# Kernel tuning notes

Hardware: AMD Instinct MI355X
Metric: run time of the kernel (lower is better)

## Reference

```python
import jax, jax.numpy as jnp
import numpy as np

EMBED_DIM = 1024
NUM_HEADS = 16
HEAD_DIM = EMBED_DIM // NUM_HEADS
B, S = 2, 2048


def setup_inputs() -> dict:
    key = jax.random.key(0)
    ks = jax.random.split(key, 11)
    glorot = lambda k, shape: jax.random.normal(k, shape, jnp.float32) * (2.0 / sum(shape)) ** 0.5
    return {
        "query": jax.random.normal(ks[0], (B, S, EMBED_DIM), jnp.float32),
        "key": jax.random.normal(ks[1], (B, S, EMBED_DIM), jnp.float32),
        "value": jax.random.normal(ks[2], (B, S, EMBED_DIM), jnp.float32),
        "Wq": glorot(ks[3], (EMBED_DIM, EMBED_DIM)), "bq": jnp.zeros((EMBED_DIM,), jnp.float32),
        "Wk": glorot(ks[4], (EMBED_DIM, EMBED_DIM)), "bk": jnp.zeros((EMBED_DIM,), jnp.float32),
        "Wv": glorot(ks[5], (EMBED_DIM, EMBED_DIM)), "bv": jnp.zeros((EMBED_DIM,), jnp.float32),
        "Wo": glorot(ks[6], (EMBED_DIM, EMBED_DIM)), "bo": jnp.zeros((EMBED_DIM,), jnp.float32),
    }


def reference(query, key, value, Wq, bq, Wk, bk, Wv, bv, Wo, bo):
    b, s, _ = query.shape
    # QKV projections
    q = query @ Wq + bq
    k = key @ Wk + bk
    v = value @ Wv + bv
    # [B, S, H, D] -> [B, H, S, D]
    q = q.reshape(b, s, NUM_HEADS, HEAD_DIM).transpose(0, 2, 1, 3)
    k = k.reshape(b, s, NUM_HEADS, HEAD_DIM).transpose(0, 2, 1, 3)
    v = v.reshape(b, s, NUM_HEADS, HEAD_DIM).transpose(0, 2, 1, 3)
    # scores [B, H, S, S], materialized as in the original
    scores = jnp.einsum("bhqd,bhkd->bhqk", q, k) / jnp.sqrt(jnp.float32(HEAD_DIM))
    attn = jax.nn.softmax(scores, axis=-1)
    out = jnp.einsum("bhqk,bhkd->bhqd", attn, v)  # [B, H, S, D]
    out = out.transpose(0, 2, 1, 3).reshape(b, s, EMBED_DIM)
    return out @ Wo + bo
```

## Files before the change

### kernel.cpp

```cpp
#include <hip/hip_runtime.h>
#include <hip/hip_bf16.h>


#define EMBED 1024
#define NHEAD 16
#define HDIM 64
#define SEQ 2048
#define MROWS 4096

typedef __attribute__((ext_vector_type(8))) __bf16 bf16x8;
typedef __attribute__((ext_vector_type(4))) float f32x4;
typedef __attribute__((ext_vector_type(16))) float f32x16;

__device__ __forceinline__ unsigned short f2bf(float f) {
  unsigned int u = __builtin_bit_cast(unsigned int, f);
  u += 0x7fffu + ((u >> 16) & 1u);
  return (unsigned short)(u >> 16);
}

__device__ __forceinline__ int cvtpk_bf16(float lo, float hi) {
  int r;
  asm("v_cvt_pk_bf16_f32 %0, %1, %2" : "=v"(r) : "v"(lo), "v"(hi));
  return r;
}

__device__ __forceinline__ float max3f(float a, float b, float c) {
  return fmaxf(fmaxf(a, b), c);
}

__device__ __forceinline__ int swz(int row, int bcol) {
  return row * 128 + (bcol ^ ((row & 7) << 4));
}

__device__ __forceinline__ void gload16(const void* g, void* l) {
  __builtin_amdgcn_global_load_lds((const __attribute__((address_space(1))) void*)g,
                                   (__attribute__((address_space(3))) void*)l, 16, 0, 0);
}

__global__ __launch_bounds__(256) void cvt_f32_bf16(const float* __restrict__ i0, const float* __restrict__ i1,
                                                    const float* __restrict__ i2,
                                                    unsigned short* __restrict__ o0, unsigned short* __restrict__ o1,
                                                    unsigned short* __restrict__ o2) {
  const float* in; unsigned short* out;
  switch (blockIdx.y) {
    case 0: in = i0; out = o0; break;
    case 1: in = i1; out = o1; break;
    default: in = i2; out = o2; break;
  }
  int i = blockIdx.x * 256 + threadIdx.x;
  const float4* p = reinterpret_cast<const float4*>(in) + (size_t)i * 2;
  float4 a = p[0], b = p[1];
  int4 r;
  r.x = cvtpk_bf16(a.x, a.y);
  r.y = cvtpk_bf16(a.z, a.w);
  r.z = cvtpk_bf16(b.x, b.y);
  r.w = cvtpk_bf16(b.z, b.w);
  reinterpret_cast<int4*>(out)[i] = r;
}

__global__ __launch_bounds__(256) void wtrans(const float* __restrict__ w0, const float* __restrict__ w1,
                                              const float* __restrict__ w2, const float* __restrict__ w3,
                                              unsigned short* __restrict__ o0, unsigned short* __restrict__ o1,
                                              unsigned short* __restrict__ o2, unsigned short* __restrict__ o3) {
  __shared__ float tile[64][65];
  const float* src; unsigned short* dst;
  switch (blockIdx.z) {
    case 0: src = w0; dst = o0; break;
    case 1: src = w1; dst = o1; break;
    case 2: src = w2; dst = o2; break;
    default: src = w3; dst = o3; break;
  }
  const int k0 = blockIdx.y * 64, n0 = blockIdx.x * 64;
  const int c = threadIdx.x & 63, r0 = threadIdx.x >> 6;
#pragma unroll
  for (int i = 0; i < 16; ++i) {
    int r = r0 + i * 4;
    tile[r][c] = src[(size_t)(k0 + r) * EMBED + n0 + c];
  }
  __syncthreads();
#pragma unroll
  for (int i = 0; i < 16; ++i) {
    int nr = r0 + i * 4;
    dst[(size_t)(n0 + nr) * EMBED + k0 + c] = f2bf(tile[c][nr]);
  }
}

template <int BN>
__device__ __forceinline__ void gemm_core(const unsigned short* __restrict__ A,
                                          const unsigned short* __restrict__ Bt,
                                          const float* __restrict__ bias,
                                          void* __restrict__ C, float oscale, int mode) {
  constexpr int K = EMBED;
  constexpr int MF = (BN == 128) ? 4 : 2;
  constexpr int BRW = BN / 4;
  __shared__ __align__(16) unsigned short Alds[128 * 64];
  __shared__ __align__(16) unsigned short Blds[BN * 64];
  char* Ab8 = (char*)Alds; char* Bb8 = (char*)Blds;
  const char* AB = (const char*)A;
  const char* BB = (const char*)Bt;
  const int tid = threadIdx.x;
  const int lane = tid & 63, w = tid >> 6;
  const int wr = (BN == 128) ? (w >> 1) : w;
  const int wc = (BN == 128) ? (w & 1) : 0;
  const int fr = lane & 15, fq = lane >> 4;
  const int m0 = blockIdx.y * 128, n0 = blockIdx.x * BN;
  const int bcol = (lane & 7) * 16;
  const int gsc = bcol ^ ((lane >> 3) << 4);

  f32x4 acc[MF][4];
#pragma unroll
  for (int m = 0; m < MF; ++m)
#pragma unroll
    for (int n = 0; n < 4; ++n) acc[m][n] = f32x4{0.f, 0.f, 0.f, 0.f};

  for (int k0 = 0; k0 < K; k0 += 64) {
    __syncthreads();
#pragma unroll
    for (int i = 0; i < 4; ++i) {
      int row = w * 32 + i * 8 + (lane >> 3);
      gload16(AB + (size_t)(m0 + row) * (K * 2) + k0 * 2 + gsc, Ab8 + w * 4096 + i * 1024);
    }
#pragma unroll
    for (int i = 0; i < BRW / 8; ++i) {
      int row = w * BRW + i * 8 + (lane >> 3);
      gload16(BB + (size_t)(n0 + row) * (K * 2) + k0 * 2 + gsc, Bb8 + w * (BRW * 128) + i * 1024);
    }
    __syncthreads();
#pragma unroll
    for (int ks = 0; ks < 2; ++ks) {
      bf16x8 af[MF], bfr[4];
#pragma unroll
      for (int m = 0; m < MF; ++m) {
        int ar = wr * (MF * 16) + m * 16 + fr;
        af[m] = *reinterpret_cast<const bf16x8*>(Ab8 + swz(ar, ks * 64 + fq * 16));
      }
#pragma unroll
      for (int n = 0; n < 4; ++n) {
        int br = wc * 64 + n * 16 + fr;
        bfr[n] = *reinterpret_cast<const bf16x8*>(Bb8 + swz(br, ks * 64 + fq * 16));
      }
#pragma unroll
      for (int m = 0; m < MF; ++m)
#pragma unroll
        for (int n = 0; n < 4; ++n)
          acc[m][n] = __builtin_amdgcn_mfma_f32_16x16x32_bf16(af[m], bfr[n], acc[m][n], 0, 0, 0);
    }
  }

#pragma unroll
  for (int n = 0; n < 4; ++n) {
    int col = n0 + wc * 64 + n * 16 + fr;
    float bv = bias[col];
#pragma unroll
    for (int m = 0; m < MF; ++m) {
      int rowb = m0 + wr * (MF * 16) + m * 16 + fq * 4;
      if (mode == 2) {
        int b = rowb >> 11, s0 = rowb & (SEQ - 1);
        int s0p = (s0 & ~12) | ((s0 & 4) << 1) | ((s0 & 8) >> 1);
        int h = col >> 6, d = col & 63;
        int2 pk;
        pk.x = cvtpk_bf16((acc[m][n][0] + bv) * oscale, (acc[m][n][1] + bv) * oscale);
        pk.y = cvtpk_bf16((acc[m][n][2] + bv) * oscale, (acc[m][n][3] + bv) * oscale);
        *reinterpret_cast<int2*>(
            &reinterpret_cast<unsigned short*>(C)[((size_t)((b * NHEAD + h) * HDIM + d)) * SEQ + s0p]) = pk;
      } else if (mode == 0) {
#pragma unroll
        for (int r = 0; r < 4; ++r) {
          int row = rowb + r;
          float v = (acc[m][n][r] + bv) * oscale;
          int b = row >> 11, s = row & (SEQ - 1), h = col >> 6, d = col & 63;
          reinterpret_cast<unsigned short*>(C)[((size_t)((b * NHEAD + h) * SEQ + s) << 6) + d] = f2bf(v);
        }
      } else {
#pragma unroll
        for (int r = 0; r < 4; ++r)
          reinterpret_cast<float*>(C)[(size_t)(rowb + r) * EMBED + col] = acc[m][n][r] + bv;
      }
    }
  }
}

__global__ __launch_bounds__(256) void gemm_qkv(
    const unsigned short* __restrict__ Xq, const unsigned short* __restrict__ Xk,
    const unsigned short* __restrict__ Xv,
    const unsigned short* __restrict__ Wqt, const unsigned short* __restrict__ Wkt,
    const unsigned short* __restrict__ Wvt,
    const float* __restrict__ bq, const float* __restrict__ bk, const float* __restrict__ bv,
    unsigned short* __restrict__ Qb, unsigned short* __restrict__ Kb,
    unsigned short* __restrict__ Vtb, float qscale) {
  switch (blockIdx.z) {
    case 0: gemm_core<128>(Xq, Wqt, bq, Qb, qscale, 0); break;
    case 1: gemm_core<128>(Xk, Wkt, bk, Kb, 1.0f, 0); break;
    default: gemm_core<128>(Xv, Wvt, bv, Vtb, 1.0f, 2); break;
  }
}

__global__ __launch_bounds__(256) void gemm_out(const unsigned short* __restrict__ A,
                                                const unsigned short* __restrict__ Bt,
                                                const float* __restrict__ bias,
                                                float* __restrict__ C) {
  gemm_core<64>(A, Bt, bias, C, 1.0f, 1);
}

__global__ __launch_bounds__(128) void attn(const unsigned short* __restrict__ Q,
                                            const unsigned short* __restrict__ Kk,
                                            const unsigned short* __restrict__ Vt,
                                            unsigned short* __restrict__ AO) {
  __shared__ __align__(16) unsigned short Klds[2][64 * 64];
  __shared__ __align__(16) unsigned short Vlds[2][64 * 64];
  const int tid = threadIdx.x, lane = tid & 63, w = tid >> 6;
  const int ql = lane & 31, t = lane >> 5;

  const int lin = blockIdx.x;
  const int head = (lin & 7) * 4 + ((lin >> 3) & 3);
  const int q0 = (lin >> 5) * 64;
  const size_t hb = (size_t)head * SEQ * HDIM;
  const unsigned short* Qh = Q + hb;
  const char* KhB = (const char*)(Kk + hb);
  const char* VhB = (const char*)(Vt + hb);

  const int gsc = ((lane & 7) * 16) ^ ((lane >> 3) << 4);
  const int row0 = w * 32 + (lane >> 3);

#define STAGE(kt_, b_)                                                                     \
  {                                                                                        \
    char* kb_ = (char*)Klds[b_];                                                           \
    char* vb_ = (char*)Vlds[b_];                                                           \
    _Pragma("unroll") for (int i_ = 0; i_ < 4; ++i_) {                                     \
      gload16(KhB + (size_t)((kt_)*64 + row0 + i_ * 8) * 128 + gsc,                        \
              kb_ + w * 4096 + i_ * 1024);                                                 \
      gload16(VhB + (size_t)(row0 + i_ * 8) * (SEQ * 2) + (kt_)*128 + gsc,                 \
              vb_ + w * 4096 + i_ * 1024);                                                 \
    }                                                                                      \
  }

  bf16x8 qf[4];
  {
    const unsigned short* qp = Qh + (size_t)(q0 + w * 32 + ql) * HDIM + t * 8;
    qf[0] = *reinterpret_cast<const bf16x8*>(qp);
    qf[1] = *reinterpret_cast<const bf16x8*>(qp + 16);
    qf[2] = *reinterpret_cast<const bf16x8*>(qp + 32);
    qf[3] = *reinterpret_cast<const bf16x8*>(qp + 48);
  }
  f32x16 oacc0 = {}, oacc1 = {};
  float mrow = -1e30f, lrow = 0.f;

  STAGE(0, 0);
  __syncthreads();

  for (int kt = 0; kt < SEQ / 64; ++kt) {
    const int cur = kt & 1;
    const bool more = (kt + 1 < SEQ / 64);
    if (more) STAGE(kt + 1, cur ^ 1);
    char* Kb8 = (char*)Klds[cur];
    char* Vb8 = (char*)Vlds[cur];

    f32x16 sc0 = {}, sc1 = {};
    __builtin_amdgcn_s_setprio(1);
#pragma unroll
    for (int s = 0; s < 4; ++s) {
      bf16x8 kf0 = *reinterpret_cast<const bf16x8*>(Kb8 + swz(ql, s * 32 + t * 16));
      bf16x8 kf1 = *reinterpret_cast<const bf16x8*>(Kb8 + swz(32 + ql, s * 32 + t * 16));
      sc0 = __builtin_amdgcn_mfma_f32_32x32x16_bf16(kf0, qf[s], sc0, 0, 0, 0);
      sc1 = __builtin_amdgcn_mfma_f32_32x32x16_bf16(kf1, qf[s], sc1, 0, 0, 0);
    }
    __builtin_amdgcn_s_setprio(0);

    float l1[12];
#pragma unroll
    for (int i = 0; i < 5; ++i) l1[i] = max3f(sc0[3 * i], sc0[3 * i + 1], sc0[3 * i + 2]);
#pragma unroll
    for (int i = 0; i < 5; ++i) l1[5 + i] = max3f(sc1[3 * i], sc1[3 * i + 1], sc1[3 * i + 2]);
    l1[10] = sc0[15];
    l1[11] = sc1[15];
    float l2a = max3f(l1[0], l1[1], l1[2]);
    float l2b = max3f(l1[3], l1[4], l1[5]);
    float l2c = max3f(l1[6], l1[7], l1[8]);
    float l2d = max3f(l1[9], l1[10], l1[11]);
    float mt = fmaxf(max3f(l2a, l2b, l2c), l2d);
    mt = fmaxf(mt, __shfl_xor(mt, 32));

    if (!__all(mt <= mrow + 8.0f)) {
      float mn = fmaxf(mrow, mt);
      float resc = __builtin_amdgcn_exp2f(mrow - mn);
      lrow *= resc;
#pragma unroll
      for (int r = 0; r < 16; ++r) {
        float rq = __shfl(resc, (r & 3) + 8 * (r >> 2) + 4 * t, 64);
        oacc0[r] *= rq;
        oacc1[r] *= rq;
      }
      mrow = mn;
    }

    float ps0 = 0.f, ps1 = 0.f, ps2 = 0.f, ps3 = 0.f;
#pragma unroll
    for (int i = 0; i < 4; ++i) {
      sc0[4 * i + 0] = __builtin_amdgcn_exp2f(sc0[4 * i + 0] - mrow);
      sc0[4 * i + 1] = __builtin_amdgcn_exp2f(sc0[4 * i + 1] - mrow);
      sc0[4 * i + 2] = __builtin_amdgcn_exp2f(sc0[4 * i + 2] - mrow);
      sc0[4 * i + 3] = __builtin_amdgcn_exp2f(sc0[4 * i + 3] - mrow);
      sc1[4 * i + 0] = __builtin_amdgcn_exp2f(sc1[4 * i + 0] - mrow);
      sc1[4 * i + 1] = __builtin_amdgcn_exp2f(sc1[4 * i + 1] - mrow);
      sc1[4 * i + 2] = __builtin_amdgcn_exp2f(sc1[4 * i + 2] - mrow);
      sc1[4 * i + 3] = __builtin_amdgcn_exp2f(sc1[4 * i + 3] - mrow);
      ps0 += sc0[4 * i + 0] + sc0[4 * i + 1];
      ps1 += sc0[4 * i + 2] + sc0[4 * i + 3];
      ps2 += sc1[4 * i + 0] + sc1[4 * i + 1];
      ps3 += sc1[4 * i + 2] + sc1[4 * i + 3];
    }
    lrow += (ps0 + ps1) + (ps2 + ps3);

    int4 paw[4];
#pragma unroll
    for (int s2 = 0; s2 < 2; ++s2) {
      paw[s2].x     = cvtpk_bf16(sc0[8 * s2 + 0], sc0[8 * s2 + 1]);
      paw[s2].y     = cvtpk_bf16(sc0[8 * s2 + 2], sc0[8 * s2 + 3]);
      paw[s2].z     = cvtpk_bf16(sc0[8 * s2 + 4], sc0[8 * s2 + 5]);
      paw[s2].w     = cvtpk_bf16(sc0[8 * s2 + 6], sc0[8 * s2 + 7]);
      paw[2 + s2].x = cvtpk_bf16(sc1[8 * s2 + 0], sc1[8 * s2 + 1]);
      paw[2 + s2].y = cvtpk_bf16(sc1[8 * s2 + 2], sc1[8 * s2 + 3]);
      paw[2 + s2].z = cvtpk_bf16(sc1[8 * s2 + 4], sc1[8 * s2 + 5]);
      paw[2 + s2].w = cvtpk_bf16(sc1[8 * s2 + 6], sc1[8 * s2 + 7]);
    }

    __builtin_amdgcn_s_setprio(1);
#pragma unroll
    for (int s = 0; s < 4; ++s) {
      bf16x8 pa = __builtin_bit_cast(bf16x8, paw[s]);
      bf16x8 v0 = *reinterpret_cast<const bf16x8*>(Vb8 + swz(ql, s * 32 + t * 16));
      bf16x8 v1 = *reinterpret_cast<const bf16x8*>(Vb8 + swz(32 + ql, s * 32 + t * 16));
      oacc0 = __builtin_amdgcn_mfma_f32_32x32x16_bf16(pa, v0, oacc0, 0, 0, 0);
      oacc1 = __builtin_amdgcn_mfma_f32_32x32x16_bf16(pa, v1, oacc1, 0, 0, 0);
    }
    __builtin_amdgcn_s_setprio(0);

    __syncthreads();
  }
#undef STAGE

  lrow += __shfl_xor(lrow, 32);

  const int b = head >> 4, hh = head & 15;
#pragma unroll
  for (int r = 0; r < 16; ++r) {
    int qr = (r & 3) + 8 * (r >> 2) + 4 * t;
    float inv = 1.0f / __shfl(lrow, qr, 64);
    int srow = q0 + w * 32 + qr;
    size_t ob = (size_t)(b * SEQ + srow) * EMBED + hh * 64 + ql;
    AO[ob] = f2bf(oacc0[r] * inv);
    AO[ob + 32] = f2bf(oacc1[r] * inv);
  }
}

extern "C" void kernel_launch(void* const* d_in, const int* in_sizes, int n_in,
                              void* d_out, int out_size, void* d_ws, size_t ws_size,
                              hipStream_t stream) {
  const float* q32 = (const float*)d_in[0];
  const float* k32 = (const float*)d_in[1];
  const float* v32 = (const float*)d_in[2];
  const float* Wq = (const float*)d_in[3]; const float* bq = (const float*)d_in[4];
  const float* Wk = (const float*)d_in[5]; const float* bk = (const float*)d_in[6];
  const float* Wv = (const float*)d_in[7]; const float* bv = (const float*)d_in[8];
  const float* Wo = (const float*)d_in[9]; const float* bo = (const float*)d_in[10];
  float* out = (float*)d_out;

  char* ws = (char*)d_ws;
  const size_t MB = 1u << 20;
  unsigned short* Xq  = (unsigned short*)(ws + 0 * MB);
  unsigned short* Xk  = (unsigned short*)(ws + 8 * MB);
  unsigned short* Xv  = (unsigned short*)(ws + 16 * MB);
  unsigned short* Wqt = (unsigned short*)(ws + 24 * MB);
  unsigned short* Wkt = (unsigned short*)(ws + 26 * MB);
  unsigned short* Wvt = (unsigned short*)(ws + 28 * MB);
  unsigned short* Wot = (unsigned short*)(ws + 30 * MB);
  unsigned short* Qb  = (unsigned short*)(ws + 32 * MB);
  unsigned short* Kb  = (unsigned short*)(ws + 40 * MB);
  unsigned short* Vtb = (unsigned short*)(ws + 48 * MB);
  unsigned short* AO  = Xq;

  const int n8 = (MROWS * EMBED) / 8;
  cvt_f32_bf16<<<dim3(n8 / 256, 3), 256, 0, stream>>>(q32, k32, v32, Xq, Xk, Xv);
  wtrans<<<dim3(16, 16, 4), 256, 0, stream>>>(Wq, Wk, Wv, Wo, Wqt, Wkt, Wvt, Wot);

  const float qscale = 0.125f * 1.44269504088896340736f;
  gemm_qkv<<<dim3(EMBED / 128, MROWS / 128, 3), 256, 0, stream>>>(
      Xq, Xk, Xv, Wqt, Wkt, Wvt, bq, bk, bv, Qb, Kb, Vtb, qscale);

  attn<<<dim3(SEQ / 64 * 32), 128, 0, stream>>>(Qb, Kb, Vtb, AO);

  gemm_out<<<dim3(EMBED / 64, MROWS / 128), 256, 0, stream>>>(AO, Wot, bo, out);
}
```

Measured before the change: 138.8 us.

## Split attention over two KV halves and merge partial outputs

The attention kernel now splits the key/value sequence into two halves along a second grid dimension. Each block writes a normalized bf16 partial output plus its running max and row sum. A new merge kernel then combines the two partials with log-sum-exp weights and writes the head-interleaved activation for the output projection. The goal is more independent blocks and shorter per-block loops to improve CU occupancy. The cost is an extra kernel launch, extra global traffic for the partials, and a second bf16 rounding of the attention output.

```diff
diff --git a/kernel.cpp b/kernel.cpp
--- a/kernel.cpp
+++ b/kernel.cpp
@@ -7,6 +7,8 @@
 #define HDIM 64
 #define SEQ 2048
 #define MROWS 4096
+#define NSPLIT 2
+#define TILES_PER_SPLIT (SEQ / 64 / NSPLIT)
 
 typedef __attribute__((ext_vector_type(8))) __bf16 bf16x8;
 typedef __attribute__((ext_vector_type(4))) float f32x4;
@@ -205,11 +207,13 @@
 __global__ __launch_bounds__(128) void attn(const unsigned short* __restrict__ Q,
                                             const unsigned short* __restrict__ Kk,
                                             const unsigned short* __restrict__ Vt,
-                                            unsigned short* __restrict__ AO) {
+                                            unsigned short* __restrict__ Po,
+                                            float2* __restrict__ Ml) {
   __shared__ __align__(16) unsigned short Klds[2][64 * 64];
   __shared__ __align__(16) unsigned short Vlds[2][64 * 64];
   const int tid = threadIdx.x, lane = tid & 63, w = tid >> 6;
   const int ql = lane & 31, t = lane >> 5;
+  const int z = blockIdx.y;
 
   const int lin = blockIdx.x;
   const int head = (lin & 7) * 4 + ((lin >> 3) & 3);
@@ -245,12 +249,13 @@
   f32x16 oacc0 = {}, oacc1 = {};
   float mrow = -1e30f, lrow = 0.f;
 
-  STAGE(0, 0);
+  const int kt0 = z * TILES_PER_SPLIT;
+  STAGE(kt0, 0);
   __syncthreads();
 
-  for (int kt = 0; kt < SEQ / 64; ++kt) {
+  for (int kt = kt0; kt < kt0 + TILES_PER_SPLIT; ++kt) {
     const int cur = kt & 1;
-    const bool more = (kt + 1 < SEQ / 64);
+    const bool more = (kt + 1 < kt0 + TILES_PER_SPLIT);
     if (more) STAGE(kt + 1, cur ^ 1);
     char* Kb8 = (char*)Klds[cur];
     char* Vb8 = (char*)Vlds[cur];
@@ -341,16 +346,42 @@
 
   lrow += __shfl_xor(lrow, 32);
 
-  const int b = head >> 4, hh = head & 15;
+  const size_t rowbase = (size_t)(z * 32 + head) * SEQ + q0 + w * 32;
+  if (t == 0) Ml[rowbase + ql] = float2{mrow, lrow};
 #pragma unroll
   for (int r = 0; r < 16; ++r) {
     int qr = (r & 3) + 8 * (r >> 2) + 4 * t;
     float inv = 1.0f / __shfl(lrow, qr, 64);
-    int srow = q0 + w * 32 + qr;
-    size_t ob = (size_t)(b * SEQ + srow) * EMBED + hh * 64 + ql;
-    AO[ob] = f2bf(oacc0[r] * inv);
-    AO[ob + 32] = f2bf(oacc1[r] * inv);
-  }
+    size_t ob = (rowbase + qr) * HDIM + ql;
+    Po[ob] = f2bf(oacc0[r] * inv);
+    Po[ob + 32] = f2bf(oacc1[r] * inv);
+  }
+}
+
+__global__ __launch_bounds__(256) void attn_merge(const unsigned int* __restrict__ Po32,
+                                                  const float2* __restrict__ Ml,
+                                                  unsigned int* __restrict__ AO32) {
+  const int idx = blockIdx.x * 256 + threadIdx.x;
+  const int row = idx >> 5;
+  const int di = idx & 31;
+  float2 ml0 = Ml[row];
+  float2 ml1 = Ml[32 * SEQ + row];
+  float M = fmaxf(ml0.x, ml1.x);
+  float a0 = __builtin_amdgcn_exp2f(ml0.x - M) * ml0.y;
+  float a1 = __builtin_amdgcn_exp2f(ml1.x - M) * ml1.y;
+  float inv = 1.0f / (a0 + a1);
+  a0 *= inv;
+  a1 *= inv;
+  unsigned int p0 = Po32[(size_t)row * 32 + di];
+  unsigned int p1 = Po32[(size_t)32 * SEQ * 32 + (size_t)row * 32 + di];
+  float lo = __builtin_bit_cast(float, (p0 & 0xffffu) << 16) * a0 +
+             __builtin_bit_cast(float, (p1 & 0xffffu) << 16) * a1;
+  float hi = __builtin_bit_cast(float, p0 & 0xffff0000u) * a0 +
+             __builtin_bit_cast(float, p1 & 0xffff0000u) * a1;
+  int head = row >> 11, srow = row & (SEQ - 1);
+  int b = head >> 4, hh = head & 15;
+  AO32[((size_t)(b * SEQ + srow) * EMBED + hh * 64) / 2 + di] =
+      (unsigned int)cvtpk_bf16(lo, hi);
 }
 
 extern "C" void kernel_launch(void* const* d_in, const int* in_sizes, int n_in,
@@ -378,6 +409,8 @@
   unsigned short* Kb  = (unsigned short*)(ws + 40 * MB);
   unsigned short* Vtb = (unsigned short*)(ws + 48 * MB);
   unsigned short* AO  = Xq;
+  unsigned short* Po  = Xk;
+  float2*         Ml  = (float2*)(ws + 24 * MB);
 
   const int n8 = (MROWS * EMBED) / 8;
   cvt_f32_bf16<<<dim3(n8 / 256, 3), 256, 0, stream>>>(q32, k32, v32, Xq, Xk, Xv);
@@ -387,7 +420,9 @@
   gemm_qkv<<<dim3(EMBED / 128, MROWS / 128, 3), 256, 0, stream>>>(
       Xq, Xk, Xv, Wqt, Wkt, Wvt, bq, bk, bv, Qb, Kb, Vtb, qscale);
 
-  attn<<<dim3(SEQ / 64 * 32), 128, 0, stream>>>(Qb, Kb, Vtb, AO);
+  attn<<<dim3(SEQ / 64 * 32, NSPLIT), 128, 0, stream>>>(Qb, Kb, Vtb, Po, Ml);
+  attn_merge<<<(32 * SEQ * 32) / 256, 256, 0, stream>>>(
+      (const unsigned int*)Po, Ml, (unsigned int*)AO);
 
   gemm_out<<<dim3(EMBED / 64, MROWS / 128), 256, 0, stream>>>(AO, Wot, bo, out);
 }
```

Result: slower. 165.2 us (+19.0%).

## Prefetch next GEMM k-tile into LDS while computing current tile from registers

Applied to the files above, without the earlier changes.

Restructures the projection GEMM main loop so each iteration reads the whole 64-wide k-slice from LDS into registers, synchronizes, then issues global-to-LDS loads for the next slice before running the MFMAs. The aim is to overlap global memory latency with matrix compute instead of stalling on a load-then-sync every iteration. The cost is higher register pressure from holding both k-substeps of fragments. It also relies on gload16 being asynchronous and correctly fenced by the next barrier.

```diff
diff --git a/kernel.cpp b/kernel.cpp
--- a/kernel.cpp
+++ b/kernel.cpp
@@ -113,39 +113,48 @@
 #pragma unroll
     for (int n = 0; n < 4; ++n) acc[m][n] = f32x4{0.f, 0.f, 0.f, 0.f};
 
+#define GSTAGE(k0_)                                                                          \
+  {                                                                                          \
+    _Pragma("unroll") for (int i_ = 0; i_ < 4; ++i_) {                                       \
+      int row_ = w * 32 + i_ * 8 + (lane >> 3);                                              \
+      gload16(AB + (size_t)(m0 + row_) * (K * 2) + (k0_)*2 + gsc, Ab8 + w * 4096 + i_ * 1024); \
+    }                                                                                        \
+    _Pragma("unroll") for (int i_ = 0; i_ < BRW / 8; ++i_) {                                 \
+      int row_ = w * BRW + i_ * 8 + (lane >> 3);                                             \
+      gload16(BB + (size_t)(n0 + row_) * (K * 2) + (k0_)*2 + gsc,                            \
+              Bb8 + w * (BRW * 128) + i_ * 1024);                                            \
+    }                                                                                        \
+  }
+
+  GSTAGE(0);
+
   for (int k0 = 0; k0 < K; k0 += 64) {
     __syncthreads();
-#pragma unroll
-    for (int i = 0; i < 4; ++i) {
-      int row = w * 32 + i * 8 + (lane >> 3);
-      gload16(AB + (size_t)(m0 + row) * (K * 2) + k0 * 2 + gsc, Ab8 + w * 4096 + i * 1024);
-    }
-#pragma unroll
-    for (int i = 0; i < BRW / 8; ++i) {
-      int row = w * BRW + i * 8 + (lane >> 3);
-      gload16(BB + (size_t)(n0 + row) * (K * 2) + k0 * 2 + gsc, Bb8 + w * (BRW * 128) + i * 1024);
-    }
-    __syncthreads();
+    bf16x8 af2[2][MF], bf2[2][4];
 #pragma unroll
     for (int ks = 0; ks < 2; ++ks) {
-      bf16x8 af[MF], bfr[4];
 #pragma unroll
       for (int m = 0; m < MF; ++m) {
         int ar = wr * (MF * 16) + m * 16 + fr;
-        af[m] = *reinterpret_cast<const bf16x8*>(Ab8 + swz(ar, ks * 64 + fq * 16));
+        af2[ks][m] = *reinterpret_cast<const bf16x8*>(Ab8 + swz(ar, ks * 64 + fq * 16));
       }
 #pragma unroll
       for (int n = 0; n < 4; ++n) {
         int br = wc * 64 + n * 16 + fr;
-        bfr[n] = *reinterpret_cast<const bf16x8*>(Bb8 + swz(br, ks * 64 + fq * 16));
+        bf2[ks][n] = *reinterpret_cast<const bf16x8*>(Bb8 + swz(br, ks * 64 + fq * 16));
       }
+    }
+    __syncthreads();
+    if (k0 + 64 < K) GSTAGE(k0 + 64);
+#pragma unroll
+    for (int ks = 0; ks < 2; ++ks)
 #pragma unroll
       for (int m = 0; m < MF; ++m)
 #pragma unroll
         for (int n = 0; n < 4; ++n)
-          acc[m][n] = __builtin_amdgcn_mfma_f32_16x16x32_bf16(af[m], bfr[n], acc[m][n], 0, 0, 0);
-    }
-  }
+          acc[m][n] = __builtin_amdgcn_mfma_f32_16x16x32_bf16(af2[ks][m], bf2[ks][n], acc[m][n], 0, 0, 0);
+  }
+#undef GSTAGE
 
 #pragma unroll
   for (int n = 0; n < 4; ++n) {
```

Result: faster. 133.5 us (-3.8%).
